# Optimization experiments

Hardware: AMD Instinct MI355X
Metric: run time of the kernel (lower is better)

The kernel has to match this reference:

```python
import jax, jax.numpy as jnp
import numpy as np

EPS = 1e-6  # eps assumed for rms/unit norm (repo uses a small eps; math identical up to eps)

def rms_norm(x):
    # normalize so RMS over last dim == 1
    return x * jax.lax.rsqrt(jnp.mean(x * x, axis=-1, keepdims=True) + EPS)

def unit_norm(w):
    # normalize each output row of the weight to unit L2 norm
    return w * jax.lax.rsqrt(jnp.sum(w * w, axis=-1, keepdims=True) + EPS)

def setup_inputs() -> dict:
    key = jax.random.key(0)
    k1, k2, k3 = jax.random.split(key, 3)
    B, S, D = 4, 2048, 2048
    x = jax.random.normal(k1, (B, S, D), dtype=jnp.float32)
    w_in = jax.random.normal(k2, (3 * D, D), dtype=jnp.float32)
    w_out = jax.random.normal(k3, (D, D), dtype=jnp.float32)
    return {"x": x, "w_in": w_in, "w_out": w_out}

def reference(x, w_in, w_out):
    B, S, D = x.shape
    H = 16
    hd = D // H
    # MPLinear in-projection with unit-normalized weight rows
    qkv = jnp.einsum("bsd,fd->bsf", x, unit_norm(w_in))  # [B,S,3D]
    qkv = qkv.reshape(B, S, 3, H, hd).transpose(2, 0, 3, 1, 4)  # [3,B,H,S,hd]
    q, k, v = qkv[0], qkv[1], qkv[2]
    q = rms_norm(q)
    k = rms_norm(k)
    # scaled dot product attention, causal, default scale 1/sqrt(hd)
    scores = jnp.einsum("bhqd,bhkd->bhqk", q, k) / jnp.sqrt(jnp.float32(hd))
    causal_mask = jnp.tril(jnp.ones((S, S), dtype=bool))
    scores = jnp.where(causal_mask, scores, jnp.finfo(scores.dtype).min)
    attn = jax.nn.softmax(scores, axis=-1)
    a = jnp.einsum("bhqk,bhkd->bhqd", attn, v)  # [B,H,S,hd]
    a = rms_norm(a)
    a = a.transpose(0, 2, 1, 3).reshape(B, S, D)
    return jnp.einsum("bsd,fd->bsf", a, unit_norm(w_out))
```

## Files before the change

kernel.cpp:

```cpp
#include <hip/hip_runtime.h>

typedef float f32x4 __attribute__((ext_vector_type(4)));
typedef __bf16 bf16x8 __attribute__((ext_vector_type(8)));

#define EPSF 1e-6f
#define AS1 __attribute__((address_space(1)))
#define AS3 __attribute__((address_space(3)))

__device__ static inline void gl_lds16(const __bf16* g, __bf16* l) {
  __builtin_amdgcn_global_load_lds((const AS1 void*)g, (AS3 void*)l, 16, 0, 0);
}

__global__ __launch_bounds__(256) void prep(const float* __restrict__ x,
                                            const float* __restrict__ w_in,
                                            const float* __restrict__ w_out,
                                            __bf16* __restrict__ xb,
                                            __bf16* __restrict__ w_in_n,
                                            __bf16* __restrict__ w_out_n) {
  __shared__ float red[4];
  const int bid = blockIdx.x;
  const int t = threadIdx.x;
  if (bid < 8192) {
    const float* src = (bid < 6144) ? (w_in + (size_t)bid * 2048)
                                    : (w_out + (size_t)(bid - 6144) * 2048);
    __bf16* dst = (bid < 6144) ? (w_in_n + (size_t)bid * 2048)
                               : (w_out_n + (size_t)(bid - 6144) * 2048);
    float4 v[2];
    float ss = 0.f;
#pragma unroll
    for (int i = 0; i < 2; i++) {
      v[i] = ((const float4*)src)[t + i * 256];
      ss += v[i].x * v[i].x + v[i].y * v[i].y + v[i].z * v[i].z + v[i].w * v[i].w;
    }
#pragma unroll
    for (int m = 32; m >= 1; m >>= 1) ss += __shfl_xor(ss, m);
    if ((t & 63) == 0) red[t >> 6] = ss;
    __syncthreads();
    float tot = red[0] + red[1] + red[2] + red[3];
    float sc = rsqrtf(tot + EPSF);
#pragma unroll
    for (int i = 0; i < 2; i++) {
      int c0 = (t + i * 256) * 4;
      dst[c0 + 0] = (__bf16)(v[i].x * sc);
      dst[c0 + 1] = (__bf16)(v[i].y * sc);
      dst[c0 + 2] = (__bf16)(v[i].z * sc);
      dst[c0 + 3] = (__bf16)(v[i].w * sc);
    }
  } else {
    size_t i = ((size_t)(bid - 8192) * 256 + t) * 8;
    float4 a = ((const float4*)(x + i))[0];
    float4 b = ((const float4*)(x + i))[1];
    bf16x8 o;
    o[0] = (__bf16)a.x; o[1] = (__bf16)a.y; o[2] = (__bf16)a.z; o[3] = (__bf16)a.w;
    o[4] = (__bf16)b.x; o[5] = (__bf16)b.y; o[6] = (__bf16)b.z; o[7] = (__bf16)b.w;
    *(bf16x8*)(xb + i) = o;
  }
}

#define LDSOFF(r_, blk_) ((r_) * 64 + (((blk_) ^ ((r_) & 7)) * 8))
#define SA(bb_, c_, kt_) gl_lds16(gA + (long)(c_) * 64 * K + (long)(kt_) * 64, &As[bb_][(c_) * 4096 + t * 8])
#define SB(bb_, c_, kt_) gl_lds16(gB + (long)(c_) * 64 * K + (long)(kt_) * 64, &Bs[bb_][(c_) * 4096 + t * 8])

template <int MODE>
__global__ __launch_bounds__(512) void gemm8(const __bf16* __restrict__ A,
                                             const __bf16* __restrict__ W,
                                             float* __restrict__ C,
                                             __bf16* __restrict__ Cb,
                                             __bf16* __restrict__ Vtb,
                                             int M, int N, int K) {
  __shared__ __bf16 As[2][16384];
  __shared__ __bf16 Bs[2][16384];
  __shared__ float rsum[8][128];

  const int gx = gridDim.x;
  const int nwg = gx * gridDim.y;
  int wg = blockIdx.y * gx + blockIdx.x;
  wg = (wg & 7) * (nwg >> 3) + (wg >> 3);
  const int bx = wg % gx, by = wg / gx;

  const int t = threadIdx.x;
  const int lane = t & 63, w = t >> 6;
  const int wr = w >> 2, wc = w & 3;
  const int wrb = wr * 128, wcb = wc * 64;
  const int fr = lane & 15, fq = lane >> 4;
  const long m0 = (long)by * 256;
  const long n0 = (long)bx * 256;
  const int NT = K >> 6;

  const int srow = t >> 3;
  const int sblk = (t & 7) ^ (srow & 7);
  const __bf16* gA = A + (m0 + srow) * (long)K + sblk * 8;
  const __bf16* gB = W + (n0 + srow) * (long)K + sblk * 8;

  f32x4 acc[8][4];
#pragma unroll
  for (int i = 0; i < 8; i++)
#pragma unroll
    for (int j = 0; j < 4; j++)
#pragma unroll
      for (int c = 0; c < 4; c++) acc[i][j][c] = 0.f;

  SA(0, 0, 0); SA(0, 1, 0); SA(0, 2, 0); SA(0, 3, 0);
  SB(0, 0, 0); SB(0, 1, 0); SB(0, 2, 0); SB(0, 3, 0);
  SA(1, 0, 1); SA(1, 2, 1);
  SB(1, 0, 1); SB(1, 1, 1); SB(1, 2, 1); SB(1, 3, 1);
  asm volatile("s_waitcnt vmcnt(6)" ::: "memory");
  __builtin_amdgcn_s_barrier();

  auto tile_step = [&](int kt, int b) {
    bf16x8 a0[4][2], b01[2][2];
#pragma unroll
    for (int i = 0; i < 4; i++)
#pragma unroll
      for (int ks = 0; ks < 2; ks++)
        a0[i][ks] = *(const bf16x8*)&As[b][LDSOFF(wrb + i * 16 + fr, ks * 4 + fq)];
#pragma unroll
    for (int j = 0; j < 2; j++)
#pragma unroll
      for (int ks = 0; ks < 2; ks++)
        b01[j][ks] = *(const bf16x8*)&Bs[b][LDSOFF(wcb + j * 16 + fr, ks * 4 + fq)];
    if (kt + 1 < NT) { SA(b ^ 1, 1, kt + 1); SA(b ^ 1, 3, kt + 1); }
    __builtin_amdgcn_s_setprio(1);
#pragma unroll
    for (int i = 0; i < 4; i++)
#pragma unroll
      for (int j = 0; j < 2; j++)
#pragma unroll
        for (int ks = 0; ks < 2; ks++)
          acc[i][j] = __builtin_amdgcn_mfma_f32_16x16x32_bf16(a0[i][ks], b01[j][ks], acc[i][j], 0, 0, 0);
    __builtin_amdgcn_s_setprio(0);
    __builtin_amdgcn_sched_barrier(0);
    __builtin_amdgcn_s_barrier();

    bf16x8 b23[2][2];
#pragma unroll
    for (int j = 0; j < 2; j++)
#pragma unroll
      for (int ks = 0; ks < 2; ks++)
        b23[j][ks] = *(const bf16x8*)&Bs[b][LDSOFF(wcb + (2 + j) * 16 + fr, ks * 4 + fq)];
    if (kt + 2 < NT) { SA(b, 0, kt + 2); SA(b, 2, kt + 2); }
    __builtin_amdgcn_s_setprio(1);
#pragma unroll
    for (int i = 0; i < 4; i++)
#pragma unroll
      for (int j = 0; j < 2; j++)
#pragma unroll
        for (int ks = 0; ks < 2; ks++)
          acc[i][2 + j] = __builtin_amdgcn_mfma_f32_16x16x32_bf16(a0[i][ks], b23[j][ks], acc[i][2 + j], 0, 0, 0);
    __builtin_amdgcn_s_setprio(0);
    __builtin_amdgcn_sched_barrier(0);
    __builtin_amdgcn_s_barrier();

    bf16x8 a1[4][2];
#pragma unroll
    for (int i = 0; i < 4; i++)
#pragma unroll
      for (int ks = 0; ks < 2; ks++)
        a1[i][ks] = *(const bf16x8*)&As[b][LDSOFF(wrb + 64 + i * 16 + fr, ks * 4 + fq)];
    if (kt + 2 < NT) { SB(b, 0, kt + 2); SB(b, 1, kt + 2); SB(b, 2, kt + 2); SB(b, 3, kt + 2); }
    __builtin_amdgcn_s_setprio(1);
#pragma unroll
    for (int i = 0; i < 4; i++)
#pragma unroll
      for (int j = 0; j < 2; j++)
#pragma unroll
        for (int ks = 0; ks < 2; ks++)
          acc[4 + i][j] = __builtin_amdgcn_mfma_f32_16x16x32_bf16(a1[i][ks], b01[j][ks], acc[4 + i][j], 0, 0, 0);
#pragma unroll
    for (int i = 0; i < 4; i++)
#pragma unroll
      for (int j = 0; j < 2; j++)
#pragma unroll
        for (int ks = 0; ks < 2; ks++)
          acc[4 + i][2 + j] = __builtin_amdgcn_mfma_f32_16x16x32_bf16(a1[i][ks], b23[j][ks], acc[4 + i][2 + j], 0, 0, 0);
    __builtin_amdgcn_s_setprio(0);
    if (kt >= NT - 2)
      asm volatile("s_waitcnt vmcnt(0)" ::: "memory");
    else
      asm volatile("s_waitcnt vmcnt(6)" ::: "memory");
    __builtin_amdgcn_sched_barrier(0);
    __builtin_amdgcn_s_barrier();
  };

  for (int kt = 0; kt < NT; kt += 2) {
    tile_step(kt, 0);
    tile_step(kt + 1, 1);
  }

  if (MODE == 0) {
#pragma unroll
    for (int i = 0; i < 8; i++)
#pragma unroll
      for (int j = 0; j < 4; j++)
#pragma unroll
        for (int r = 0; r < 4; r++) {
          long row = m0 + wrb + i * 16 + fq * 4 + r;
          long col = n0 + wcb + j * 16 + fr;
          C[row * N + col] = acc[i][j][r];
        }
  } else {
    const int tt = (int)(n0 >> 11);
    const int hh = (int)(((n0 >> 7) + (wc >> 1)) & 15);
    const long e0 = (long)(wc & 1) * 64;
    if (tt < 2) {
#pragma unroll
      for (int i = 0; i < 8; i++)
#pragma unroll
        for (int r = 0; r < 4; r++) {
          float s2 = 0.f;
#pragma unroll
          for (int j = 0; j < 4; j++) s2 += acc[i][j][r] * acc[i][j][r];
          s2 += __shfl_xor(s2, 1);
          s2 += __shfl_xor(s2, 2);
          s2 += __shfl_xor(s2, 4);
          s2 += __shfl_xor(s2, 8);
          if (fr == 0) rsum[w][i * 16 + fq * 4 + r] = s2;
        }
      __syncthreads();
#pragma unroll
      for (int i = 0; i < 8; i++)
#pragma unroll
        for (int r = 0; r < 4; r++) {
          int rl = i * 16 + fq * 4 + r;
          float tot = rsum[w][rl] + rsum[w ^ 1][rl];
          float sc = rsqrtf(tot * (1.f / 128.f) + EPSF);
          long row = m0 + wrb + rl;
          long bb = row >> 11, ss = row & 2047;
          __bf16* base = Cb + ((((long)tt * 4 + bb) * 16 + hh) * 2048 + ss) * 128 + e0;
#pragma unroll
          for (int j = 0; j < 4; j++)
            base[j * 16 + fr] = (__bf16)(acc[i][j][r] * sc);
        }
    } else {
#pragma unroll
      for (int i = 0; i < 8; i++)
#pragma unroll
        for (int r = 0; r < 4; r++) {
          long row = m0 + wrb + i * 16 + fq * 4 + r;
          long bb = row >> 11, ss = row & 2047;
#pragma unroll
          for (int j = 0; j < 4; j++)
            Vtb[((bb * 16 + hh) * 128 + e0 + j * 16 + fr) * 2048 + ss] = (__bf16)acc[i][j][r];
        }
    }
  }
}

__global__ __launch_bounds__(256, 3) void attn(const __bf16* __restrict__ qkv,
                                               const __bf16* __restrict__ vt,
                                               __bf16* __restrict__ an) {
  __shared__ __bf16 Ks[64 * 128];
  __shared__ __bf16 Vs[128 * 64];
  __shared__ __bf16 plds[8][16 * 40];
  const int L = blockIdx.x;
  const int qt = L >> 6;
  const int bh = (L & 7) + 8 * ((L >> 3) & 7);
  const int t = threadIdx.x;
  const int lane = t & 63, w = t >> 6;
  const int fr = lane & 15, fq = lane >> 4;
  const int swz = fr & 7;
  const __bf16* Q = qkv + (long)bh * 262144;
  const __bf16* Kbh = qkv + 16777216L + (long)bh * 262144;
  const __bf16* Vbh = vt + (long)bh * 262144;
  const float sc2 = 0.08838834764831845f * 1.4426950408889634f;
  const float MFIX = 20.0f;
  const int b = bh >> 4, h = bh & 15;

  const __bf16* gK = Kbh + (long)(t >> 4) * 128 + ((t & 15) ^ ((t >> 4) & 7)) * 8;
  const __bf16* gV = Vbh + (long)(t >> 3) * 2048 + ((t & 7) ^ ((t >> 3) & 7)) * 8;
  __bf16* lK = &Ks[t * 8];
  __bf16* lV = &Vs[t * 8];

#pragma unroll 1
  for (int side = 0; side < 2; side++) {
    const int qi = side ? (15 - qt) : qt;
    const int q0 = qi * 128 + w * 32;
    const int cha = q0 >> 5;
    bf16x8 qf[2][4];
#pragma unroll
    for (int f = 0; f < 2; f++)
#pragma unroll
      for (int ec = 0; ec < 4; ec++)
        qf[f][ec] = *(const bf16x8*)(Q + (long)(q0 + f * 16 + fr) * 128 + ec * 32 + fq * 8);
    float lacc[2][4];
#pragma unroll
    for (int f = 0; f < 2; f++)
#pragma unroll
      for (int r = 0; r < 4; r++) lacc[f][r] = 0.f;
    f32x4 oacc[2][8];
#pragma unroll
    for (int f = 0; f < 2; f++)
#pragma unroll
      for (int e = 0; e < 8; e++)
#pragma unroll
        for (int c = 0; c < 4; c++) oacc[f][e][c] = 0.f;

    const int nst = 2 * qi + 2;
#pragma unroll 1
    for (int st = 0; st < nst; st++) {
      const long k0 = (long)st * 64;
#pragma unroll
      for (int j = 0; j < 4; j++) gl_lds16(gK + (k0 + j * 16) * 128, lK + j * 2048);
#pragma unroll
      for (int j = 0; j < 4; j++) gl_lds16(gV + (long)j * 32 * 2048 + k0, lV + j * 2048);
      __syncthreads();
#pragma unroll
      for (int half = 0; half < 2; half++) {
        const int k32 = (int)k0 + half * 32;
        const int ch = k32 >> 5;
        if (ch <= cha) {
          f32x4 sa[2][2];
#pragma unroll
          for (int f = 0; f < 2; f++)
#pragma unroll
            for (int ct = 0; ct < 2; ct++)
#pragma unroll
              for (int c = 0; c < 4; c++) sa[f][ct][c] = 0.f;
#pragma unroll
          for (int ct = 0; ct < 2; ct++) {
#pragma unroll
            for (int ec = 0; ec < 4; ec++) {
              bf16x8 kf = *(const bf16x8*)(&Ks[(half * 32 + ct * 16 + fr) * 128 +
                                               ((ec * 4 + fq) ^ swz) * 8]);
              sa[0][ct] = __builtin_amdgcn_mfma_f32_16x16x32_bf16(qf[0][ec], kf, sa[0][ct], 0, 0, 0);
              sa[1][ct] = __builtin_amdgcn_mfma_f32_16x16x32_bf16(qf[1][ec], kf, sa[1][ct], 0, 0, 0);
            }
          }
#pragma unroll
          for (int f = 0; f < 2; f++) {
            __bf16* pwf = plds[(w << 1) + f];
            if (ch == cha) {
#pragma unroll
              for (int r = 0; r < 4; r++) {
                int qg = q0 + f * 16 + fq * 4 + r;
                float p0 = exp2f(((k32 + fr) <= qg) ? sa[f][0][r] * sc2 - MFIX : -1e30f);
                float p1 = exp2f(((k32 + 16 + fr) <= qg) ? sa[f][1][r] * sc2 - MFIX : -1e30f);
                lacc[f][r] += p0 + p1;
                pwf[(fq * 4 + r) * 40 + fr] = (__bf16)p0;
                pwf[(fq * 4 + r) * 40 + 16 + fr] = (__bf16)p1;
              }
            } else {
#pragma unroll
              for (int r = 0; r < 4; r++) {
                float p0 = exp2f(__builtin_fmaf(sa[f][0][r], sc2, -MFIX));
                float p1 = exp2f(__builtin_fmaf(sa[f][1][r], sc2, -MFIX));
                lacc[f][r] += p0 + p1;
                pwf[(fq * 4 + r) * 40 + fr] = (__bf16)p0;
                pwf[(fq * 4 + r) * 40 + 16 + fr] = (__bf16)p1;
              }
            }
          }
          bf16x8 pa0 = *(const bf16x8*)(&plds[(w << 1) + 0][fr * 40 + fq * 8]);
          bf16x8 pa1 = *(const bf16x8*)(&plds[(w << 1) + 1][fr * 40 + fq * 8]);
#pragma unroll
          for (int e = 0; e < 8; e++) {
            bf16x8 vf = *(const bf16x8*)(&Vs[(e * 16 + fr) * 64 +
                                             ((half * 4 + fq) ^ swz) * 8]);
            oacc[0][e] = __builtin_amdgcn_mfma_f32_16x16x32_bf16(pa0, vf, oacc[0][e], 0, 0, 0);
            oacc[1][e] = __builtin_amdgcn_mfma_f32_16x16x32_bf16(pa1, vf, oacc[1][e], 0, 0, 0);
          }
        }
      }
      __syncthreads();
    }
#pragma unroll
    for (int f = 0; f < 2; f++)
#pragma unroll
      for (int r = 0; r < 4; r++) {
        float ls = lacc[f][r];
        ls += __shfl_xor(ls, 1);
        ls += __shfl_xor(ls, 2);
        ls += __shfl_xor(ls, 4);
        ls += __shfl_xor(ls, 8);
        float inv = 1.0f / ls;
        float ssq = 0.f;
#pragma unroll
        for (int e = 0; e < 8; e++) { float v = oacc[f][e][r] * inv; ssq += v * v; }
        ssq += __shfl_xor(ssq, 1);
        ssq += __shfl_xor(ssq, 2);
        ssq += __shfl_xor(ssq, 4);
        ssq += __shfl_xor(ssq, 8);
        float rsc = rsqrtf(ssq * (1.f / 128.f) + EPSF) * inv;
        long s = q0 + f * 16 + fq * 4 + r;
        __bf16* dst = an + ((long)b * 2048 + s) * 2048 + h * 128;
#pragma unroll
        for (int e = 0; e < 8; e++) dst[e * 16 + fr] = (__bf16)(oacc[f][e][r] * rsc);
      }
  }
}

extern "C" void kernel_launch(void* const* d_in, const int* in_sizes, int n_in,
                              void* d_out, int out_size, void* d_ws, size_t ws_size,
                              hipStream_t stream) {
  const float* x = (const float*)d_in[0];
  const float* w_in = (const float*)d_in[1];
  const float* w_out = (const float*)d_in[2];
  float* out = (float*)d_out;
  char* ws = (char*)d_ws;

  __bf16* w_in_n = (__bf16*)(ws);
  __bf16* w_out_n = (__bf16*)(ws + 25165824);
  __bf16* xb = (__bf16*)(ws + 33554432);
  __bf16* an = xb;
  __bf16* qkv = (__bf16*)(ws + 67108864);
  __bf16* vt = (__bf16*)(ws + 167772160);

  prep<<<16384, 256, 0, stream>>>(x, w_in, w_out, xb, w_in_n, w_out_n);
  gemm8<1><<<dim3(24, 32), 512, 0, stream>>>(xb, w_in_n, nullptr, qkv, vt, 8192, 6144, 2048);
  attn<<<512, 256, 0, stream>>>(qkv, vt, an);
  gemm8<0><<<dim3(8, 32), 512, 0, stream>>>(an, w_out_n, out, nullptr, nullptr, 8192, 2048, 2048);
}
```

Baseline: 517.9 us.

## Split prep into separate kernels, split QKV GEMM launch, add MFMA priority hints

The fused prep kernel becomes two kernels: norm_w, which normalizes the weight rows and now writes them with vectorized bf16x4 stores, and cast_x, which converts x to bf16. The QKV in-projection GEMM is split into two launches covering columns 0-4095 and 4096-6143, using a new nbase column offset. In the attention kernel, s_setprio is raised around the QK and PV MFMA blocks to favour matrix work over other waves. These are several loosely related tweaks that add kernel launches and may affect tail balance, with the split GEMM possibly changing the wave quantization.

```diff
diff --git a/kernel.cpp b/kernel.cpp
--- a/kernel.cpp
+++ b/kernel.cpp
@@ -2,6 +2,7 @@
 
 typedef float f32x4 __attribute__((ext_vector_type(4)));
 typedef __bf16 bf16x8 __attribute__((ext_vector_type(8)));
+typedef __bf16 bf16x4 __attribute__((ext_vector_type(4)));
 
 #define EPSF 1e-6f
 #define AS1 __attribute__((address_space(1)))
@@ -11,50 +12,50 @@
   __builtin_amdgcn_global_load_lds((const AS1 void*)g, (AS3 void*)l, 16, 0, 0);
 }
 
-__global__ __launch_bounds__(256) void prep(const float* __restrict__ x,
-                                            const float* __restrict__ w_in,
-                                            const float* __restrict__ w_out,
-                                            __bf16* __restrict__ xb,
-                                            __bf16* __restrict__ w_in_n,
-                                            __bf16* __restrict__ w_out_n) {
+__global__ __launch_bounds__(256) void norm_w(const float* __restrict__ w_in,
+                                              const float* __restrict__ w_out,
+                                              __bf16* __restrict__ w_in_n,
+                                              __bf16* __restrict__ w_out_n) {
   __shared__ float red[4];
-  const int bid = blockIdx.x;
+  const int row = blockIdx.x;
+  const float* src = (row < 6144) ? (w_in + (size_t)row * 2048)
+                                  : (w_out + (size_t)(row - 6144) * 2048);
+  __bf16* dst = (row < 6144) ? (w_in_n + (size_t)row * 2048)
+                             : (w_out_n + (size_t)(row - 6144) * 2048);
   const int t = threadIdx.x;
-  if (bid < 8192) {
-    const float* src = (bid < 6144) ? (w_in + (size_t)bid * 2048)
-                                    : (w_out + (size_t)(bid - 6144) * 2048);
-    __bf16* dst = (bid < 6144) ? (w_in_n + (size_t)bid * 2048)
-                               : (w_out_n + (size_t)(bid - 6144) * 2048);
-    float4 v[2];
-    float ss = 0.f;
-#pragma unroll
-    for (int i = 0; i < 2; i++) {
-      v[i] = ((const float4*)src)[t + i * 256];
-      ss += v[i].x * v[i].x + v[i].y * v[i].y + v[i].z * v[i].z + v[i].w * v[i].w;
-    }
-#pragma unroll
-    for (int m = 32; m >= 1; m >>= 1) ss += __shfl_xor(ss, m);
-    if ((t & 63) == 0) red[t >> 6] = ss;
-    __syncthreads();
-    float tot = red[0] + red[1] + red[2] + red[3];
-    float sc = rsqrtf(tot + EPSF);
-#pragma unroll
-    for (int i = 0; i < 2; i++) {
-      int c0 = (t + i * 256) * 4;
-      dst[c0 + 0] = (__bf16)(v[i].x * sc);
-      dst[c0 + 1] = (__bf16)(v[i].y * sc);
-      dst[c0 + 2] = (__bf16)(v[i].z * sc);
-      dst[c0 + 3] = (__bf16)(v[i].w * sc);
-    }
-  } else {
-    size_t i = ((size_t)(bid - 8192) * 256 + t) * 8;
-    float4 a = ((const float4*)(x + i))[0];
-    float4 b = ((const float4*)(x + i))[1];
-    bf16x8 o;
-    o[0] = (__bf16)a.x; o[1] = (__bf16)a.y; o[2] = (__bf16)a.z; o[3] = (__bf16)a.w;
-    o[4] = (__bf16)b.x; o[5] = (__bf16)b.y; o[6] = (__bf16)b.z; o[7] = (__bf16)b.w;
-    *(bf16x8*)(xb + i) = o;
+  float4 v[2];
+  float ss = 0.f;
+#pragma unroll
+  for (int i = 0; i < 2; i++) {
+    v[i] = ((const float4*)src)[t + i * 256];
+    ss += v[i].x * v[i].x + v[i].y * v[i].y + v[i].z * v[i].z + v[i].w * v[i].w;
   }
+#pragma unroll
+  for (int m = 32; m >= 1; m >>= 1) ss += __shfl_xor(ss, m);
+  if ((t & 63) == 0) red[t >> 6] = ss;
+  __syncthreads();
+  float tot = red[0] + red[1] + red[2] + red[3];
+  float sc = rsqrtf(tot + EPSF);
+#pragma unroll
+  for (int i = 0; i < 2; i++) {
+    bf16x4 o;
+    o[0] = (__bf16)(v[i].x * sc);
+    o[1] = (__bf16)(v[i].y * sc);
+    o[2] = (__bf16)(v[i].z * sc);
+    o[3] = (__bf16)(v[i].w * sc);
+    *(bf16x4*)(dst + (t + i * 256) * 4) = o;
+  }
+}
+
+__global__ __launch_bounds__(256) void cast_x(const float* __restrict__ x,
+                                              __bf16* __restrict__ xb) {
+  size_t i = ((size_t)blockIdx.x * 256 + threadIdx.x) * 8;
+  float4 a = ((const float4*)(x + i))[0];
+  float4 b = ((const float4*)(x + i))[1];
+  bf16x8 o;
+  o[0] = (__bf16)a.x; o[1] = (__bf16)a.y; o[2] = (__bf16)a.z; o[3] = (__bf16)a.w;
+  o[4] = (__bf16)b.x; o[5] = (__bf16)b.y; o[6] = (__bf16)b.z; o[7] = (__bf16)b.w;
+  *(bf16x8*)(xb + i) = o;
 }
 
 #define LDSOFF(r_, blk_) ((r_) * 64 + (((blk_) ^ ((r_) & 7)) * 8))
@@ -67,7 +68,7 @@
                                              float* __restrict__ C,
                                              __bf16* __restrict__ Cb,
                                              __bf16* __restrict__ Vtb,
-                                             int M, int N, int K) {
+                                             int nbase, int M, int N, int K) {
   __shared__ __bf16 As[2][16384];
   __shared__ __bf16 Bs[2][16384];
   __shared__ float rsum[8][128];
@@ -84,7 +85,7 @@
   const int wrb = wr * 128, wcb = wc * 64;
   const int fr = lane & 15, fq = lane >> 4;
   const long m0 = (long)by * 256;
-  const long n0 = (long)bx * 256;
+  const long n0 = (long)nbase + (long)bx * 256;
   const int NT = K >> 6;
 
   const int srow = t >> 3;
@@ -316,6 +317,7 @@
             for (int ct = 0; ct < 2; ct++)
 #pragma unroll
               for (int c = 0; c < 4; c++) sa[f][ct][c] = 0.f;
+          __builtin_amdgcn_s_setprio(1);
 #pragma unroll
           for (int ct = 0; ct < 2; ct++) {
 #pragma unroll
@@ -326,6 +328,7 @@
               sa[1][ct] = __builtin_amdgcn_mfma_f32_16x16x32_bf16(qf[1][ec], kf, sa[1][ct], 0, 0, 0);
             }
           }
+          __builtin_amdgcn_s_setprio(0);
 #pragma unroll
           for (int f = 0; f < 2; f++) {
             __bf16* pwf = plds[(w << 1) + f];
@@ -352,6 +355,7 @@
           }
           bf16x8 pa0 = *(const bf16x8*)(&plds[(w << 1) + 0][fr * 40 + fq * 8]);
           bf16x8 pa1 = *(const bf16x8*)(&plds[(w << 1) + 1][fr * 40 + fq * 8]);
+          __builtin_amdgcn_s_setprio(1);
 #pragma unroll
           for (int e = 0; e < 8; e++) {
             bf16x8 vf = *(const bf16x8*)(&Vs[(e * 16 + fr) * 64 +
@@ -359,6 +363,7 @@
             oacc[0][e] = __builtin_amdgcn_mfma_f32_16x16x32_bf16(pa0, vf, oacc[0][e], 0, 0, 0);
             oacc[1][e] = __builtin_amdgcn_mfma_f32_16x16x32_bf16(pa1, vf, oacc[1][e], 0, 0, 0);
           }
+          __builtin_amdgcn_s_setprio(0);
         }
       }
       __syncthreads();
@@ -405,8 +410,10 @@
   __bf16* qkv = (__bf16*)(ws + 67108864);
   __bf16* vt = (__bf16*)(ws + 167772160);
 
-  prep<<<16384, 256, 0, stream>>>(x, w_in, w_out, xb, w_in_n, w_out_n);
-  gemm8<1><<<dim3(24, 32), 512, 0, stream>>>(xb, w_in_n, nullptr, qkv, vt, 8192, 6144, 2048);
+  norm_w<<<8192, 256, 0, stream>>>(w_in, w_out, w_in_n, w_out_n);
+  cast_x<<<8192, 256, 0, stream>>>(x, xb);
+  gemm8<1><<<dim3(16, 32), 512, 0, stream>>>(xb, w_in_n, nullptr, qkv, vt, 0, 8192, 6144, 2048);
+  gemm8<1><<<dim3(8, 32), 512, 0, stream>>>(xb, w_in_n, nullptr, qkv, vt, 4096, 8192, 6144, 2048);
   attn<<<512, 256, 0, stream>>>(qkv, vt, an);
-  gemm8<0><<<dim3(8, 32), 512, 0, stream>>>(an, w_out_n, out, nullptr, nullptr, 8192, 2048, 2048);
-}
+  gemm8<0><<<dim3(8, 32), 512, 0, stream>>>(an, w_out_n, out, nullptr, nullptr, 0, 8192, 2048, 2048);
+}
```

Measured after the change: 524.4 us. About the same (+1.2%).
